# Kernel optimization log

Measured on AMD Instinct MI355X. Metric: run time of the kernel, lower is better.

Reference implementation:

```python
import jax, jax.numpy as jnp
import numpy as np
import math

N = 100000      # nodes
E = 1600000     # edges
D = 128         # in_channels
C = 256         # number of dominant-set cliques
HID = 64        # mlp_hidden
RATIO = 0.8
K = int(math.ceil(RATIO * N))  # 80000 topk nodes per view


def setup_inputs() -> dict:
    key = jax.random.key(0)
    ks = jax.random.split(key, 18)
    s = 0.05
    return {
        "x": jax.random.normal(ks[0], (N, D), jnp.float32),
        "edge_index": jax.random.randint(ks[1], (2, E), 0, N, dtype=jnp.int32),
        "batch": jnp.zeros((N,), jnp.int32),
        "cluster_id": jax.random.randint(ks[2], (N,), 0, C, dtype=jnp.int32),
        # MLP scorer: Linear(D,HID) -> ReLU -> Linear(HID,1)
        "mlp_w1": jax.random.normal(ks[3], (D, HID), jnp.float32) * s,
        "mlp_b1": jnp.zeros((HID,), jnp.float32),
        "mlp_w2": jax.random.normal(ks[4], (HID, 1), jnp.float32) * s,
        "mlp_b2": jnp.zeros((1,), jnp.float32),
        # GATConv(D, 1, heads=1)
        "gat_w": jax.random.normal(ks[5], (D, 1), jnp.float32) * s,
        "gat_a_src": jax.random.normal(ks[6], (1,), jnp.float32) * s,
        "gat_a_dst": jax.random.normal(ks[7], (1,), jnp.float32) * s,
        "gat_b": jnp.zeros((1,), jnp.float32),
        # InterChannelGCN attention Linear(2D,1) split into fine/coarse halves
        "att_w_fine": jax.random.normal(ks[8], (D,), jnp.float32) * s,
        "att_w_coarse": jax.random.normal(ks[9], (D,), jnp.float32) * s,
        "att_b": jnp.zeros((1,), jnp.float32),
        # InterChannelGCN transform Linear(D,D)
        "trans_w": jax.random.normal(ks[10], (D, D), jnp.float32) * s,
        "trans_b": jnp.zeros((D,), jnp.float32),
    }


def _inter_channel_gcn(h_fine, H_coarse, R, wa, wb, ab, tw, tb):
    # attention(Linear(2D,1)) on concat(h_fine_i, H_coarse_j) == h_fine@wa + H_coarse@wb + b
    scores = h_fine @ wa[:, None] + (H_coarse @ wb)[None, :] + ab[0]   # [K, C]
    attn = jax.nn.softmax(scores * R, axis=-1)                          # mask-by-multiply, as original
    out = attn @ H_coarse + h_fine                                      # add_self=True
    return jax.nn.relu(out @ tw + tb)                                   # normalize=False


def reference(x, edge_index, batch, cluster_id,
              mlp_w1, mlp_b1, mlp_w2, mlp_b2,
              gat_w, gat_a_src, gat_a_dst, gat_b,
              att_w_fine, att_w_coarse, att_b, trans_w, trans_b):
    src, dst = edge_index[0], edge_index[1]

    # --- DominantClustering('avg'): cluster means as coarse features ---
    counts = jax.ops.segment_sum(jnp.ones((N,), jnp.float32), cluster_id, num_segments=C)
    Hcoarse = jax.ops.segment_sum(x, cluster_id, num_segments=C) / jnp.maximum(counts, 1.0)[:, None]

    # --- feature view: MLP score + topk ---
    feature_score = (jax.nn.relu(x @ mlp_w1 + mlp_b1) @ mlp_w2 + mlp_b2)[:, 0]   # [N]
    _, feat_idx = jax.lax.top_k(feature_score, K)
    feature_view3 = x[feat_idx]
    R_feat = jax.nn.one_hot(cluster_id[feat_idx], C, dtype=x.dtype)              # relationship matrix
    fuse1 = _inter_channel_gcn(feature_view3, Hcoarse, R_feat,
                               att_w_fine, att_w_coarse, att_b, trans_w, trans_b)

    # --- local view: GATConv(D,1,heads=1) score + topk ---
    h = x @ gat_w                                                                 # [N,1]
    e = jax.nn.leaky_relu(gat_a_src[0] * h[src, 0] + gat_a_dst[0] * h[dst, 0], 0.2)  # [E]
    m = jax.ops.segment_max(e, dst, num_segments=N)
    ex = jnp.exp(e - m[dst])
    den = jax.ops.segment_sum(ex, dst, num_segments=N)
    alpha = ex / jnp.maximum(den[dst], 1e-16)
    localview_score = jax.ops.segment_sum(alpha * h[src, 0], dst, num_segments=N) + gat_b[0]
    _, local_idx = jax.lax.top_k(localview_score, K)
    local_view1 = x[local_idx]
    R_local = jax.nn.one_hot(cluster_id[local_idx], C, dtype=x.dtype)
    fuse2 = _inter_channel_gcn(local_view1, Hcoarse, R_local,
                               att_w_fine, att_w_coarse, att_b, trans_w, trans_b)

    # --- union, edge filtering + remapping (padded fixed shapes) ---
    in_feat = jnp.zeros((N,), bool).at[feat_idx].set(True)
    in_local = jnp.zeros((N,), bool).at[local_idx].set(True)
    union = in_feat | in_local
    mapping = jnp.where(union, jnp.cumsum(union.astype(jnp.int32)) - 1, -1)
    m0, m1 = mapping[src], mapping[dst]
    valid = (m0 >= 0) & (m1 >= 0)
    edge_index_topk = jnp.where(valid[None, :], jnp.stack([m0, m1]), -1)          # [2,E], -1 = dropped

    # --- fused features (faithful to original's fuse1/fuse2 index swap) ---
    A = jnp.zeros((N, D), x.dtype).at[feat_idx].set(fuse2)    # fuse2 indexed by feature topk position
    B = jnp.zeros((N, D), x.dtype).at[local_idx].set(fuse1)   # fuse1 indexed by local topk position
    both = in_feat & in_local
    Fp = jnp.where(both[:, None], (A + B) * 0.5, A + B)
    Fp = jnp.where(union[:, None], Fp, 0.0)                   # [N,D], zero outside union

    new_batch = jnp.where(union, batch, -1)
    return Fp, edge_index_topk, new_batch
```

## Files before the change

kernel.cpp:

```cpp
#include <hip/hip_runtime.h>
#include <hip/hip_bf16.h>
#include <stdint.h>

#define N 100000
#define E_ 1600000
#define D 128
#define C_ 256
#define HID 64
#define KSEL 80000
#define NB 4096
#define CHUNK 1024
#define NCHUNK ((N + CHUNK - 1) / CHUNK)
#define CSEG 32
#define NBK 782
#define BCAP 2560
#define RMAX 2048

__device__ __forceinline__ unsigned enc_f(float f) {
  unsigned b = __float_as_uint(f);
  return (b & 0x80000000u) ? ~b : (b | 0x80000000u);
}
__device__ __forceinline__ float dec_f(unsigned u) {
  unsigned b = (u & 0x80000000u) ? (u ^ 0x80000000u) : ~u;
  return __uint_as_float(b);
}

__global__ __launch_bounds__(256) void k_hist_cluster(const int* __restrict__ cid, int* __restrict__ ccount) {
  int n = blockIdx.x * 256 + threadIdx.x;
  if (n < N) atomicAdd(&ccount[cid[n]], 1);
}

__global__ __launch_bounds__(1024) void k_scan_small(const int* __restrict__ in0, int* __restrict__ out0, int n) {
  __shared__ int sums[1024];
  const int* in = in0 + (size_t)blockIdx.x * n;
  int* out = out0 + (size_t)blockIdx.x * n;
  int t = threadIdx.x;
  int per = (n + 1023) / 1024;
  int base = t * per;
  int loc = 0;
  for (int k = 0; k < per; ++k) { int i = base + k; if (i < n) loc += in[i]; }
  sums[t] = loc; __syncthreads();
  for (int off = 1; off < 1024; off <<= 1) {
    int v = (t >= off) ? sums[t - off] : 0;
    __syncthreads();
    sums[t] += v;
    __syncthreads();
  }
  int run = (t == 0) ? 0 : sums[t - 1];
  for (int k = 0; k < per; ++k) { int i = base + k; if (i < n) { out[i] = run; run += in[i]; } }
}

__global__ __launch_bounds__(256) void k_scatter_cluster(const int* __restrict__ cid, const int* __restrict__ cstart,
                                                         int* __restrict__ ccur, int* __restrict__ cslot) {
  int n = blockIdx.x * 256 + threadIdx.x;
  if (n < N) {
    int c = cid[n];
    int p = cstart[c] + atomicAdd(&ccur[c], 1);
    cslot[p] = n;
  }
}

__global__ __launch_bounds__(128) void k_cluster_partial(const float* __restrict__ x, const int* __restrict__ cstart,
                                                         const int* __restrict__ ccount, const int* __restrict__ cslot,
                                                         float* __restrict__ Hc) {
  int c = blockIdx.x >> 5;
  int s = blockIdx.x & (CSEG - 1);
  int d = threadIdx.x;
  int st = cstart[c], cnt = ccount[c];
  int seg = (cnt + CSEG - 1) / CSEG;
  int lo = s * seg;
  int hi = min(cnt, lo + seg);
  if (lo >= hi) return;
  float acc = 0.f;
  int k = lo;
  for (; k + 2 <= hi; k += 2) {
    int n0 = cslot[st + k], n1 = cslot[st + k + 1];
    float v0 = x[(size_t)n0 * D + d];
    float v1 = x[(size_t)n1 * D + d];
    acc += v0 + v1;
  }
  if (k < hi) acc += x[(size_t)cslot[st + k] * D + d];
  atomicAdd(&Hc[(size_t)c * D + d], acc);
}

__global__ __launch_bounds__(128) void k_mean_gdot(const int* __restrict__ ccount, const float* __restrict__ wb,
                                                   float* __restrict__ Hc, float* __restrict__ gdot) {
  __shared__ float red[128];
  int c = blockIdx.x, d = threadIdx.x;
  float hv = Hc[(size_t)c * D + d] / (float)max(ccount[c], 1);
  Hc[(size_t)c * D + d] = hv;
  red[d] = hv * wb[d];
  __syncthreads();
  if (d < 64) {
    float v = red[d] + red[d + 64];
    for (int off = 32; off; off >>= 1) v += __shfl_down(v, off);
    if (d == 0) gdot[c] = v;
  }
}

__global__ __launch_bounds__(128) void k_S_SW_HW(const float* __restrict__ Hc, const float* __restrict__ tw,
                                                 float* __restrict__ SW, float* __restrict__ HW) {
  __shared__ float Sl[128];
  int b = blockIdx.x, t = threadIdx.x;
  if (b == 0) {
    float s = 0.f;
    for (int c = 0; c < C_; ++c) s += Hc[(size_t)c * D + t];
    Sl[t] = s;
    __syncthreads();
    float acc = 0.f;
    for (int d = 0; d < D; ++d) acc = fmaf(Sl[d], tw[(size_t)d * D + t], acc);
    SW[t] = acc;
  } else {
    const float* src = Hc + (size_t)(b - 1) * D;
    float acc = 0.f;
    for (int d = 0; d < D; ++d) acc = fmaf(src[d], tw[(size_t)d * D + t], acc);
    HW[(size_t)(b - 1) * D + t] = acc;
  }
}

__global__ __launch_bounds__(256, 4) void k_score64(const float* __restrict__ x, const float* __restrict__ w1,
                                                    const float* __restrict__ b1, const float* __restrict__ w2,
                                                    const float* __restrict__ b2, const float* __restrict__ gw,
                                                    const float* __restrict__ wa, float* __restrict__ scoreF,
                                                    float* __restrict__ hg, float* __restrict__ aDot) {
  __shared__ float xld[64 * D];
  int tid = threadIdx.x;
  int base = blockIdx.x * 64;
#pragma unroll
  for (int k = 0; k < 8; ++k) {
    int i = k * 256 + tid;
    int r = i >> 5, off = i & 31;
    int n = base + r;
    float4 v = make_float4(0.f, 0.f, 0.f, 0.f);
    if (n < N) v = ((const float4*)(x + (size_t)n * D))[off];
    ((float4*)xld)[i] = v;
  }
  __syncthreads();

  int rg = tid >> 5;
  int cg = tid & 31;
  int c2 = cg * 2;
  float acc[8][2] = {};
  const float* xb = xld + rg * 8 * D;
  for (int d4 = 0; d4 < D; d4 += 4) {
    float2 wv0 = *(const float2*)(w1 + (size_t)(d4 + 0) * HID + c2);
    float2 wv1 = *(const float2*)(w1 + (size_t)(d4 + 1) * HID + c2);
    float2 wv2 = *(const float2*)(w1 + (size_t)(d4 + 2) * HID + c2);
    float2 wv3 = *(const float2*)(w1 + (size_t)(d4 + 3) * HID + c2);
#pragma unroll
    for (int r = 0; r < 8; ++r) {
      float4 xv = *(const float4*)(xb + r * D + d4);
      acc[r][0] = fmaf(xv.x, wv0.x, acc[r][0]);
      acc[r][1] = fmaf(xv.x, wv0.y, acc[r][1]);
      acc[r][0] = fmaf(xv.y, wv1.x, acc[r][0]);
      acc[r][1] = fmaf(xv.y, wv1.y, acc[r][1]);
      acc[r][0] = fmaf(xv.z, wv2.x, acc[r][0]);
      acc[r][1] = fmaf(xv.z, wv2.y, acc[r][1]);
      acc[r][0] = fmaf(xv.w, wv3.x, acc[r][0]);
      acc[r][1] = fmaf(xv.w, wv3.y, acc[r][1]);
    }
  }
  float2 b1v = *(const float2*)(b1 + c2);
  float2 w2v = *(const float2*)(w2 + c2);
  float bb = b2[0];
#pragma unroll
  for (int r = 0; r < 8; ++r) {
    float p = fmaxf(acc[r][0] + b1v.x, 0.f) * w2v.x + fmaxf(acc[r][1] + b1v.y, 0.f) * w2v.y;
#pragma unroll
    for (int off = 16; off; off >>= 1) p += __shfl_xor(p, off);
    if (cg == 0) {
      int n = base + rg * 8 + r;
      if (n < N) scoreF[n] = p + bb;
    }
  }
  float4 gwv = *(const float4*)(gw + cg * 4);
  float4 wav = *(const float4*)(wa + cg * 4);
#pragma unroll
  for (int r = 0; r < 8; ++r) {
    int row = rg * 8 + r;
    float4 xv = *(const float4*)(xld + row * D + cg * 4);
    float hp = xv.x * gwv.x + xv.y * gwv.y + xv.z * gwv.z + xv.w * gwv.w;
    float ap = xv.x * wav.x + xv.y * wav.y + xv.z * wav.z + xv.w * wav.w;
#pragma unroll
    for (int off = 16; off; off >>= 1) {
      hp += __shfl_xor(hp, off);
      ap += __shfl_xor(ap, off);
    }
    if (cg == 0) {
      int n = base + row;
      if (n < N) { hg[n] = hp; aDot[n] = ap; }
    }
  }
}

__global__ __launch_bounds__(1024) void k_escatter(const int* __restrict__ ei, const float* __restrict__ hg,
                                                   const float* __restrict__ asrc, const float* __restrict__ adst,
                                                   int* __restrict__ gcnt, uint2* __restrict__ payload) {
  __shared__ int lcnt[NBK];
  __shared__ int lbase[NBK];
  int tid = threadIdx.x;
  for (int i = tid; i < NBK; i += 1024) lcnt[i] = 0;
  int e0 = blockIdx.x * 8192;
  int es[8], ed[8];
#pragma unroll
  for (int k = 0; k < 8; ++k) {
    int e = e0 + k * 1024 + tid;
    bool v = (e < E_);
    es[k] = v ? ei[e] : -1;
    ed[k] = v ? ei[E_ + e] : -1;
  }
  __syncthreads();
#pragma unroll
  for (int k = 0; k < 8; ++k)
    if (ed[k] >= 0) atomicAdd(&lcnt[ed[k] >> 7], 1);
  __syncthreads();
  for (int i = tid; i < NBK; i += 1024) {
    int c = lcnt[i];
    lbase[i] = c ? atomicAdd(&gcnt[i], c) : 0;
    lcnt[i] = 0;
  }
  __syncthreads();
  float as = asrc[0], ad = adst[0];
#pragma unroll
  for (int k = 0; k < 8; ++k) {
    if (ed[k] < 0) continue;
    int s = es[k], d = ed[k];
    int b = d >> 7, dl = d & 127;
    float z = as * hg[s] + ad * hg[d];
    float ev = (z > 0.f) ? z : 0.2f * z;
    int pos = lbase[b] + atomicAdd(&lcnt[b], 1);
    if (pos < BCAP) {
      uint2 rec;
      rec.x = __float_as_uint(ev);
      rec.y = (unsigned)s | ((unsigned)dl << 24);
      payload[(size_t)b * BCAP + pos] = rec;
    }
  }
}

__global__ __launch_bounds__(256) void k_esoftmax(const uint2* __restrict__ payload, const int* __restrict__ gcnt,
                                                  const float* __restrict__ hg, const float* __restrict__ gb,
                                                  float* __restrict__ scoreL) {
  __shared__ unsigned mS[128];
  __shared__ float dS[128];
  __shared__ float nS[128];
  int b = blockIdx.x;
  int tid = threadIdx.x;
  if (tid < 128) { mS[tid] = 0u; dS[tid] = 0.f; nS[tid] = 0.f; }
  __syncthreads();
  int cnt = min(gcnt[b], BCAP);
  const uint2* bp = payload + (size_t)b * BCAP;
  for (int i = tid; i < cnt; i += 256) {
    uint2 r = bp[i];
    atomicMax(&mS[r.y >> 24], enc_f(__uint_as_float(r.x)));
  }
  __syncthreads();
  for (int i = tid; i < cnt; i += 256) {
    uint2 r = bp[i];
    int d = r.y >> 24;
    float ex = expf(__uint_as_float(r.x) - dec_f(mS[d]));
    atomicAdd(&dS[d], ex);
  }
  __syncthreads();
  for (int i = tid; i < cnt; i += 256) {
    uint2 r = bp[i];
    int d = r.y >> 24;
    float ex = expf(__uint_as_float(r.x) - dec_f(mS[d]));
    float alpha = ex / fmaxf(dS[d], 1e-16f);
    float h = hg[r.y & 0xFFFFFFu];
    atomicAdd(&nS[d], alpha * h);
  }
  __syncthreads();
  if (tid < 128) {
    int dst = b * 128 + tid;
    if (dst < N) scoreL[dst] = nS[tid] + gb[0];
  }
}

__global__ __launch_bounds__(256) void k_minmax2(const float* __restrict__ sc2, unsigned* __restrict__ mm) {
  __shared__ unsigned smx[256], smn[256];
  int v = blockIdx.y;
  const float* sc = sc2 + (size_t)v * N;
  int t = threadIdx.x; int n = blockIdx.x * 256 + t;
  unsigned val = (n < N) ? enc_f(sc[n]) : 0u;
  smx[t] = (n < N) ? val : 0u;
  smn[t] = (n < N) ? val : 0xFFFFFFFFu;
  __syncthreads();
  for (int off = 128; off; off >>= 1) {
    if (t < off) {
      smx[t] = max(smx[t], smx[t + off]);
      smn[t] = min(smn[t], smn[t + off]);
    }
    __syncthreads();
  }
  if (t == 0) { atomicMax(&mm[v], smx[0]); atomicMin(&mm[2 + v], smn[0]); }
}

__global__ __launch_bounds__(256) void k_bucket_hist2(const float* __restrict__ sc2, const unsigned* __restrict__ mm,
                                                      int* __restrict__ bucket2, int* __restrict__ hist2) {
  int v = blockIdx.y;
  int n = blockIdx.x * 256 + threadIdx.x;
  if (n >= N) return;
  const float* sc = sc2 + (size_t)v * N;
  float smax = dec_f(mm[v]), smin = dec_f(mm[2 + v]);
  float range = smax - smin;
  float scale = (range > 0.f) ? ((float)NB / range) : 0.f;
  float t = (smax - sc[n]) * scale;
  int b = (int)t;
  b = b < 0 ? 0 : (b > NB - 1 ? NB - 1 : b);
  bucket2[(size_t)v * N + n] = b;
  atomicAdd(&hist2[v * NB + b], 1);
}

__global__ __launch_bounds__(256) void k_bucket_scatter2(const int* __restrict__ bucket2, const int* __restrict__ start2,
                                                         int* __restrict__ cur2, int* __restrict__ slot2) {
  int v = blockIdx.y;
  int n = blockIdx.x * 256 + threadIdx.x;
  if (n >= N) return;
  int b = bucket2[(size_t)v * N + n];
  slot2[(size_t)v * N + start2[v * NB + b] + atomicAdd(&cur2[v * NB + b], 1)] = n;
}

__global__ __launch_bounds__(64) void k_bucket_rank3(const float* __restrict__ sc2, const int* __restrict__ start2,
                                                     const int* __restrict__ hist2, const int* __restrict__ slot2,
                                                     int* __restrict__ rank2, int* __restrict__ sorted2) {
  __shared__ unsigned long long keys[RMAX];
  int v = blockIdx.y;
  int b = blockIdx.x;
  int st = start2[v * NB + b], cnt = hist2[v * NB + b];
  if (cnt == 0) return;
  const float* sc = sc2 + (size_t)v * N;
  const int* slot = slot2 + (size_t)v * N;
  int* rank = rank2 + (size_t)v * N;
  int* sorted = sorted2 + (size_t)v * N;
  int tid = threadIdx.x;
  if (cnt <= RMAX) {
    for (int i = tid; i < cnt; i += 64) {
      int m = slot[st + i];
      keys[i] = (((unsigned long long)(~enc_f(sc[m]))) << 32) | (unsigned)m;
    }
    __syncthreads();
    for (int i = tid; i < cnt; i += 64) {
      unsigned long long mykey = keys[i];
      int r = 0;
      for (int j = 0; j < cnt; ++j) r += (keys[j] < mykey) ? 1 : 0;
      int m = (int)(mykey & 0xFFFFFFFFu);
      rank[m] = st + r;
      sorted[st + r] = m;
    }
  } else {
    for (int i = tid; i < cnt; i += 64) {
      int m = slot[st + i];
      unsigned long long mykey = (((unsigned long long)(~enc_f(sc[m]))) << 32) | (unsigned)m;
      int r = 0;
      for (int j = 0; j < cnt; ++j) {
        int mj = slot[st + j];
        unsigned long long k = (((unsigned long long)(~enc_f(sc[mj]))) << 32) | (unsigned)mj;
        r += (k < mykey) ? 1 : 0;
      }
      rank[m] = st + r;
      sorted[st + r] = m;
    }
  }
}

__global__ __launch_bounds__(1024) void k_union_chunksum(const int* __restrict__ rankF, const int* __restrict__ rankL,
                                                         int* __restrict__ csum) {
  __shared__ int red[1024];
  int t = threadIdx.x; int i = blockIdx.x * 1024 + t;
  int u = (i < N) ? (((rankF[i] < KSEL) || (rankL[i] < KSEL)) ? 1 : 0) : 0;
  red[t] = u; __syncthreads();
  for (int off = 512; off; off >>= 1) { if (t < off) red[t] += red[t + off]; __syncthreads(); }
  if (t == 0) csum[blockIdx.x] = red[0];
}

__global__ __launch_bounds__(1024) void k_union_map(const int* __restrict__ rankF, const int* __restrict__ rankL,
                                                    const int* __restrict__ cstart, const int* __restrict__ batch,
                                                    int* __restrict__ mapping, float* __restrict__ outBatch) {
  __shared__ int sums[1024];
  int t = threadIdx.x; int i = blockIdx.x * 1024 + t;
  int u = (i < N) ? (((rankF[i] < KSEL) || (rankL[i] < KSEL)) ? 1 : 0) : 0;
  sums[t] = u; __syncthreads();
  for (int off = 1; off < 1024; off <<= 1) {
    int v = (t >= off) ? sums[t - off] : 0;
    __syncthreads();
    sums[t] += v;
    __syncthreads();
  }
  if (i < N) {
    mapping[i] = u ? (cstart[blockIdx.x] + sums[t] - 1) : -1;
    outBatch[i] = u ? (float)batch[i] : -1.0f;
  }
}

__global__ __launch_bounds__(256) void k_edge_out(const int* __restrict__ ei, const int* __restrict__ mapping,
                                                  float* __restrict__ outE) {
  int e = blockIdx.x * 256 + threadIdx.x;
  if (e >= E_) return;
  int m0 = mapping[ei[e]], m1 = mapping[ei[E_ + e]];
  bool valid = (m0 >= 0) && (m1 >= 0);
  outE[e] = valid ? (float)m0 : -1.f;
  outE[E_ + e] = valid ? (float)m1 : -1.f;
}

__global__ __launch_bounds__(128, 2) void k_fuse64(const float* __restrict__ x, const float* __restrict__ tw,
                                                   const float* __restrict__ tb, const float* __restrict__ SW,
                                                   const float* __restrict__ HW, const float* __restrict__ gdot,
                                                   const float* __restrict__ aDot, const int* __restrict__ cid,
                                                   const int* __restrict__ srcL, const int* __restrict__ tgtL,
                                                   const float* __restrict__ attb, const int* __restrict__ rankF,
                                                   float* __restrict__ Fp, int accum) {
  __shared__ float xld[64 * D];
  __shared__ float pq[64 * 2];
  __shared__ int mt[64 * 2];
  int tid = threadIdx.x;
  int base = blockIdx.x * 64;
  if (tid < 64) {
    int ws = srcL[base + tid];
    int cc = cid[ws];
    mt[tid * 2] = cc;
    mt[tid * 2 + 1] = tgtL[base + tid];
    float s = aDot[ws] + gdot[cc] + attb[0];
    float mx = fmaxf(s, 0.f);
    float esm = expf(s - mx), eom = expf(-mx);
    float dn = esm + 255.f * eom;
    pq[tid * 2] = esm / dn;
    pq[tid * 2 + 1] = eom / dn;
  }
#pragma unroll
  for (int k = 0; k < 16; ++k) {
    int i = k * 128 + tid;
    int r = i >> 5, off = i & 31;
    int ws = srcL[base + r];
    ((float4*)xld)[i] = ((const float4*)(x + (size_t)ws * D))[off];
  }
  __syncthreads();

  int rg = tid >> 4;
  int cg = tid & 15;
  int c8 = cg * 8;
  float acc[8][8] = {};
  const float* xb = xld + rg * 8 * D;
  for (int d4 = 0; d4 < D; d4 += 4) {
    float tww[4][8];
#pragma unroll
    for (int dd = 0; dd < 4; ++dd) {
      *(float4*)&tww[dd][0] = *(const float4*)(tw + (size_t)(d4 + dd) * D + c8);
      *(float4*)&tww[dd][4] = *(const float4*)(tw + (size_t)(d4 + dd) * D + c8 + 4);
    }
#pragma unroll
    for (int r = 0; r < 8; ++r) {
      float4 xv = *(const float4*)(xb + r * D + d4);
      float xs[4] = {xv.x, xv.y, xv.z, xv.w};
#pragma unroll
      for (int dd = 0; dd < 4; ++dd)
#pragma unroll
        for (int c = 0; c < 8; ++c)
          acc[r][c] = fmaf(xs[dd], tww[dd][c], acc[r][c]);
    }
  }

  float4 tb0 = *(const float4*)(tb + c8);
  float4 tb1 = *(const float4*)(tb + c8 + 4);
  float4 sw0 = *(const float4*)(SW + c8);
  float4 sw1 = *(const float4*)(SW + c8 + 4);
#pragma unroll
  for (int r = 0; r < 8; ++r) {
    int row = rg * 8 + r;
    float p = pq[row * 2], q = pq[row * 2 + 1];
    int cc = mt[row * 2];
    int tgt = mt[row * 2 + 1];
    float4 hw0 = *(const float4*)(HW + (size_t)cc * D + c8);
    float4 hw1 = *(const float4*)(HW + (size_t)cc * D + c8 + 4);
    float4 o0, o1;
    o0.x = fmaxf(acc[r][0] + tb0.x + q * sw0.x + (p - q) * hw0.x, 0.f);
    o0.y = fmaxf(acc[r][1] + tb0.y + q * sw0.y + (p - q) * hw0.y, 0.f);
    o0.z = fmaxf(acc[r][2] + tb0.z + q * sw0.z + (p - q) * hw0.z, 0.f);
    o0.w = fmaxf(acc[r][3] + tb0.w + q * sw0.w + (p - q) * hw0.w, 0.f);
    o1.x = fmaxf(acc[r][4] + tb1.x + q * sw1.x + (p - q) * hw1.x, 0.f);
    o1.y = fmaxf(acc[r][5] + tb1.y + q * sw1.y + (p - q) * hw1.y, 0.f);
    o1.z = fmaxf(acc[r][6] + tb1.z + q * sw1.z + (p - q) * hw1.z, 0.f);
    o1.w = fmaxf(acc[r][7] + tb1.w + q * sw1.w + (p - q) * hw1.w, 0.f);
    float4* dst0 = (float4*)(Fp + (size_t)tgt * D + c8);
    float4* dst1 = (float4*)(Fp + (size_t)tgt * D + c8 + 4);
    if (accum) {
      float4 a0 = *dst0, a1 = *dst1;
      o0.x += a0.x; o0.y += a0.y; o0.z += a0.z; o0.w += a0.w;
      o1.x += a1.x; o1.y += a1.y; o1.z += a1.z; o1.w += a1.w;
      if (rankF[tgt] < KSEL) {
        o0.x *= 0.5f; o0.y *= 0.5f; o0.z *= 0.5f; o0.w *= 0.5f;
        o1.x *= 0.5f; o1.y *= 0.5f; o1.z *= 0.5f; o1.w *= 0.5f;
      }
    }
    *dst0 = o0;
    *dst1 = o1;
  }
}

extern "C" void kernel_launch(void* const* d_in, const int* in_sizes, int n_in,
                              void* d_out, int out_size, void* d_ws, size_t ws_size,
                              hipStream_t stream) {
  const float* x   = (const float*)d_in[0];
  const int* ei    = (const int*)d_in[1];
  const int* batch = (const int*)d_in[2];
  const int* cid   = (const int*)d_in[3];
  const float* w1  = (const float*)d_in[4];
  const float* b1  = (const float*)d_in[5];
  const float* w2  = (const float*)d_in[6];
  const float* b2  = (const float*)d_in[7];
  const float* gw  = (const float*)d_in[8];
  const float* gas = (const float*)d_in[9];
  const float* gad = (const float*)d_in[10];
  const float* gb  = (const float*)d_in[11];
  const float* wa  = (const float*)d_in[12];
  const float* wb  = (const float*)d_in[13];
  const float* ab  = (const float*)d_in[14];
  const float* tw  = (const float*)d_in[15];
  const float* tb  = (const float*)d_in[16];
  (void)in_sizes; (void)n_in; (void)ws_size; (void)out_size;

  char* p = (char*)d_ws;
  auto alloc = [&](size_t bytes) -> char* {
    char* r = p;
    p += (bytes + 255) & ~(size_t)255;
    return r;
  };
  int* ccount    = (int*)alloc(C_ * 4);
  int* ccur      = (int*)alloc(C_ * 4);
  unsigned* mm   = (unsigned*)alloc(16);
  int* hist2     = (int*)alloc(2 * NB * 4);
  int* cur2      = (int*)alloc(2 * NB * 4);
  float* Hc      = (float*)alloc((size_t)C_ * D * 4);
  int* gcnt      = (int*)alloc(NBK * 4);
  size_t zeroBytes = (size_t)(p - (char*)d_ws);
  int* cstart   = (int*)alloc(C_ * 4);
  int* cslot    = (int*)alloc((size_t)N * 4);
  float* gdot   = (float*)alloc(C_ * 4);
  float* SW     = (float*)alloc(D * 4);
  float* HW     = (float*)alloc((size_t)C_ * D * 4);
  float* score2 = (float*)alloc((size_t)2 * N * 4);
  float* hg     = (float*)alloc((size_t)N * 4);
  float* aDot   = (float*)alloc((size_t)N * 4);
  uint2* payload = (uint2*)alloc((size_t)NBK * BCAP * 8);
  int* bucket2  = (int*)alloc((size_t)2 * N * 4);
  int* start2   = (int*)alloc(2 * NB * 4);
  int* slot2    = (int*)alloc((size_t)2 * N * 4);
  int* sorted2  = (int*)alloc((size_t)2 * N * 4);
  int* rank2    = (int*)alloc((size_t)2 * N * 4);
  int* csums    = (int*)alloc(NCHUNK * 4);
  int* cstarts  = (int*)alloc(NCHUNK * 4);
  int* mapping  = (int*)alloc((size_t)N * 4);

  float* scoreF = score2;
  float* scoreL = score2 + N;
  int* sortedF  = sorted2;
  int* sortedL  = sorted2 + N;
  int* rankF    = rank2;
  int* rankL    = rank2 + N;

  float* outF = (float*)d_out;
  float* outE = outF + (size_t)N * D;
  float* outB = outE + (size_t)2 * E_;

  hipMemsetAsync(d_ws, 0, zeroBytes, stream);
  hipMemsetAsync(outF, 0, (size_t)N * D * 4, stream);
  hipMemsetAsync(mm + 2, 0xFF, 8, stream);

  k_hist_cluster<<<(N + 255) / 256, 256, 0, stream>>>(cid, ccount);
  k_scan_small<<<1, 1024, 0, stream>>>(ccount, cstart, C_);
  k_scatter_cluster<<<(N + 255) / 256, 256, 0, stream>>>(cid, cstart, ccur, cslot);
  k_cluster_partial<<<C_ * CSEG, 128, 0, stream>>>(x, cstart, ccount, cslot, Hc);
  k_mean_gdot<<<C_, 128, 0, stream>>>(ccount, wb, Hc, gdot);
  k_S_SW_HW<<<C_ + 1, 128, 0, stream>>>(Hc, tw, SW, HW);

  k_score64<<<(N + 63) / 64, 256, 0, stream>>>(x, w1, b1, w2, b2, gw, wa, scoreF, hg, aDot);
  k_escatter<<<(E_ + 8191) / 8192, 1024, 0, stream>>>(ei, hg, gas, gad, gcnt, payload);
  k_esoftmax<<<NBK, 256, 0, stream>>>(payload, gcnt, hg, gb, scoreL);

  dim3 g2((N + 255) / 256, 2);
  k_minmax2<<<g2, 256, 0, stream>>>(score2, mm);
  k_bucket_hist2<<<g2, 256, 0, stream>>>(score2, mm, bucket2, hist2);
  k_scan_small<<<2, 1024, 0, stream>>>(hist2, start2, NB);
  k_bucket_scatter2<<<g2, 256, 0, stream>>>(bucket2, start2, cur2, slot2);
  dim3 gr(NB, 2);
  k_bucket_rank3<<<gr, 64, 0, stream>>>(score2, start2, hist2, slot2, rank2, sorted2);

  k_union_chunksum<<<NCHUNK, 1024, 0, stream>>>(rankF, rankL, csums);
  k_scan_small<<<1, 1024, 0, stream>>>(csums, cstarts, NCHUNK);
  k_union_map<<<NCHUNK, 1024, 0, stream>>>(rankF, rankL, cstarts, batch, mapping, outB);
  k_edge_out<<<(E_ + 255) / 256, 256, 0, stream>>>(ei, mapping, outE);

  k_fuse64<<<KSEL / 64, 128, 0, stream>>>(x, tw, tb, SW, HW, gdot, aDot, cid, sortedL, sortedF, ab, rankF, outF, 0);
  k_fuse64<<<KSEL / 64, 128, 0, stream>>>(x, tw, tb, SW, HW, gdot, aDot, cid, sortedF, sortedL, ab, rankF, outF, 1);
}
```

Before: 589.2 us.

## Zero only non-union rows and retile fuse kernel to 256 threads

The full memset of the feature output is replaced by a small kernel that zeroes only rows outside the union, since union rows are fully overwritten by the two fuse passes. The second fuse pass now reads back the previous row only for nodes present in both views, and precomputes that flag in shared memory. The fuse GEMM moves from 128 threads with 8x8 tiles to 256 threads with 8x4 tiles, with register double-buffering of the transform weights. This saves output bandwidth but adds a launch, and the smaller tiles load the weights more times per output.

```diff
diff --git a/kernel.cpp b/kernel.cpp
--- a/kernel.cpp
+++ b/kernel.cpp
@@ -403,7 +403,13 @@
   outE[E_ + e] = valid ? (float)m1 : -1.f;
 }
 
-__global__ __launch_bounds__(128, 2) void k_fuse64(const float* __restrict__ x, const float* __restrict__ tw,
+__global__ __launch_bounds__(256) void k_zero_rows(const int* __restrict__ mapping, float* __restrict__ Fp) {
+  int i = blockIdx.x * 256 + threadIdx.x;
+  int n = i >> 5;
+  if (n < N && mapping[n] < 0) ((float4*)Fp)[i] = make_float4(0.f, 0.f, 0.f, 0.f);
+}
+
+__global__ __launch_bounds__(256, 4) void k_fuse64(const float* __restrict__ x, const float* __restrict__ tw,
                                                    const float* __restrict__ tb, const float* __restrict__ SW,
                                                    const float* __restrict__ HW, const float* __restrict__ gdot,
                                                    const float* __restrict__ aDot, const int* __restrict__ cid,
@@ -413,13 +419,16 @@
   __shared__ float xld[64 * D];
   __shared__ float pq[64 * 2];
   __shared__ int mt[64 * 2];
+  __shared__ int ft[64];
   int tid = threadIdx.x;
   int base = blockIdx.x * 64;
   if (tid < 64) {
     int ws = srcL[base + tid];
     int cc = cid[ws];
+    int tg = tgtL[base + tid];
     mt[tid * 2] = cc;
-    mt[tid * 2 + 1] = tgtL[base + tid];
+    mt[tid * 2 + 1] = tg;
+    ft[tid] = (rankF[tg] < KSEL) ? 1 : 0;
     float s = aDot[ws] + gdot[cc] + attb[0];
     float mx = fmaxf(s, 0.f);
     float esm = expf(s - mx), eom = expf(-mx);
@@ -428,72 +437,78 @@
     pq[tid * 2 + 1] = eom / dn;
   }
 #pragma unroll
-  for (int k = 0; k < 16; ++k) {
-    int i = k * 128 + tid;
+  for (int k = 0; k < 8; ++k) {
+    int i = k * 256 + tid;
     int r = i >> 5, off = i & 31;
     int ws = srcL[base + r];
     ((float4*)xld)[i] = ((const float4*)(x + (size_t)ws * D))[off];
   }
   __syncthreads();
 
-  int rg = tid >> 4;
-  int cg = tid & 15;
-  int c8 = cg * 8;
-  float acc[8][8] = {};
+  int rg = tid >> 5;
+  int c4 = (tid & 31) * 4;
+  float acc[8][4] = {};
   const float* xb = xld + rg * 8 * D;
+  float4 t0 = *(const float4*)(tw + (size_t)0 * D + c4);
+  float4 t1 = *(const float4*)(tw + (size_t)1 * D + c4);
+  float4 t2 = *(const float4*)(tw + (size_t)2 * D + c4);
+  float4 t3 = *(const float4*)(tw + (size_t)3 * D + c4);
   for (int d4 = 0; d4 < D; d4 += 4) {
-    float tww[4][8];
-#pragma unroll
-    for (int dd = 0; dd < 4; ++dd) {
-      *(float4*)&tww[dd][0] = *(const float4*)(tw + (size_t)(d4 + dd) * D + c8);
-      *(float4*)&tww[dd][4] = *(const float4*)(tw + (size_t)(d4 + dd) * D + c8 + 4);
+    float4 u0, u1, u2, u3;
+    if (d4 + 4 < D) {
+      u0 = *(const float4*)(tw + (size_t)(d4 + 4) * D + c4);
+      u1 = *(const float4*)(tw + (size_t)(d4 + 5) * D + c4);
+      u2 = *(const float4*)(tw + (size_t)(d4 + 6) * D + c4);
+      u3 = *(const float4*)(tw + (size_t)(d4 + 7) * D + c4);
+    } else {
+      u0 = u1 = u2 = u3 = make_float4(0.f, 0.f, 0.f, 0.f);
     }
 #pragma unroll
     for (int r = 0; r < 8; ++r) {
       float4 xv = *(const float4*)(xb + r * D + d4);
-      float xs[4] = {xv.x, xv.y, xv.z, xv.w};
-#pragma unroll
-      for (int dd = 0; dd < 4; ++dd)
-#pragma unroll
-        for (int c = 0; c < 8; ++c)
-          acc[r][c] = fmaf(xs[dd], tww[dd][c], acc[r][c]);
-    }
-  }
-
-  float4 tb0 = *(const float4*)(tb + c8);
-  float4 tb1 = *(const float4*)(tb + c8 + 4);
-  float4 sw0 = *(const float4*)(SW + c8);
-  float4 sw1 = *(const float4*)(SW + c8 + 4);
+      acc[r][0] = fmaf(xv.x, t0.x, acc[r][0]);
+      acc[r][1] = fmaf(xv.x, t0.y, acc[r][1]);
+      acc[r][2] = fmaf(xv.x, t0.z, acc[r][2]);
+      acc[r][3] = fmaf(xv.x, t0.w, acc[r][3]);
+      acc[r][0] = fmaf(xv.y, t1.x, acc[r][0]);
+      acc[r][1] = fmaf(xv.y, t1.y, acc[r][1]);
+      acc[r][2] = fmaf(xv.y, t1.z, acc[r][2]);
+      acc[r][3] = fmaf(xv.y, t1.w, acc[r][3]);
+      acc[r][0] = fmaf(xv.z, t2.x, acc[r][0]);
+      acc[r][1] = fmaf(xv.z, t2.y, acc[r][1]);
+      acc[r][2] = fmaf(xv.z, t2.z, acc[r][2]);
+      acc[r][3] = fmaf(xv.z, t2.w, acc[r][3]);
+      acc[r][0] = fmaf(xv.w, t3.x, acc[r][0]);
+      acc[r][1] = fmaf(xv.w, t3.y, acc[r][1]);
+      acc[r][2] = fmaf(xv.w, t3.z, acc[r][2]);
+      acc[r][3] = fmaf(xv.w, t3.w, acc[r][3]);
+    }
+    t0 = u0; t1 = u1; t2 = u2; t3 = u3;
+  }
+
+  float4 tbv = *(const float4*)(tb + c4);
+  float4 swv = *(const float4*)(SW + c4);
 #pragma unroll
   for (int r = 0; r < 8; ++r) {
     int row = rg * 8 + r;
     float p = pq[row * 2], q = pq[row * 2 + 1];
     int cc = mt[row * 2];
     int tgt = mt[row * 2 + 1];
-    float4 hw0 = *(const float4*)(HW + (size_t)cc * D + c8);
-    float4 hw1 = *(const float4*)(HW + (size_t)cc * D + c8 + 4);
-    float4 o0, o1;
-    o0.x = fmaxf(acc[r][0] + tb0.x + q * sw0.x + (p - q) * hw0.x, 0.f);
-    o0.y = fmaxf(acc[r][1] + tb0.y + q * sw0.y + (p - q) * hw0.y, 0.f);
-    o0.z = fmaxf(acc[r][2] + tb0.z + q * sw0.z + (p - q) * hw0.z, 0.f);
-    o0.w = fmaxf(acc[r][3] + tb0.w + q * sw0.w + (p - q) * hw0.w, 0.f);
-    o1.x = fmaxf(acc[r][4] + tb1.x + q * sw1.x + (p - q) * hw1.x, 0.f);
-    o1.y = fmaxf(acc[r][5] + tb1.y + q * sw1.y + (p - q) * hw1.y, 0.f);
-    o1.z = fmaxf(acc[r][6] + tb1.z + q * sw1.z + (p - q) * hw1.z, 0.f);
-    o1.w = fmaxf(acc[r][7] + tb1.w + q * sw1.w + (p - q) * hw1.w, 0.f);
-    float4* dst0 = (float4*)(Fp + (size_t)tgt * D + c8);
-    float4* dst1 = (float4*)(Fp + (size_t)tgt * D + c8 + 4);
-    if (accum) {
-      float4 a0 = *dst0, a1 = *dst1;
-      o0.x += a0.x; o0.y += a0.y; o0.z += a0.z; o0.w += a0.w;
-      o1.x += a1.x; o1.y += a1.y; o1.z += a1.z; o1.w += a1.w;
-      if (rankF[tgt] < KSEL) {
-        o0.x *= 0.5f; o0.y *= 0.5f; o0.z *= 0.5f; o0.w *= 0.5f;
-        o1.x *= 0.5f; o1.y *= 0.5f; o1.z *= 0.5f; o1.w *= 0.5f;
-      }
-    }
-    *dst0 = o0;
-    *dst1 = o1;
+    float4 hw = *(const float4*)(HW + (size_t)cc * D + c4);
+    float4 o;
+    o.x = fmaxf(acc[r][0] + tbv.x + q * swv.x + (p - q) * hw.x, 0.f);
+    o.y = fmaxf(acc[r][1] + tbv.y + q * swv.y + (p - q) * hw.y, 0.f);
+    o.z = fmaxf(acc[r][2] + tbv.z + q * swv.z + (p - q) * hw.z, 0.f);
+    o.w = fmaxf(acc[r][3] + tbv.w + q * swv.w + (p - q) * hw.w, 0.f);
+    float4* dst = (float4*)(Fp + (size_t)tgt * D + c4);
+    if (accum && ft[row]) {
+      float4 old = *dst;
+      o.x = (o.x + old.x) * 0.5f;
+      o.y = (o.y + old.y) * 0.5f;
+      o.z = (o.z + old.z) * 0.5f;
+      o.w = (o.w + old.w) * 0.5f;
+    }
+    *dst = o;
   }
 }
 
@@ -563,7 +578,6 @@
   float* outB = outE + (size_t)2 * E_;
 
   hipMemsetAsync(d_ws, 0, zeroBytes, stream);
-  hipMemsetAsync(outF, 0, (size_t)N * D * 4, stream);
   hipMemsetAsync(mm + 2, 0xFF, 8, stream);
 
   k_hist_cluster<<<(N + 255) / 256, 256, 0, stream>>>(cid, ccount);
@@ -589,7 +603,8 @@
   k_scan_small<<<1, 1024, 0, stream>>>(csums, cstarts, NCHUNK);
   k_union_map<<<NCHUNK, 1024, 0, stream>>>(rankF, rankL, cstarts, batch, mapping, outB);
   k_edge_out<<<(E_ + 255) / 256, 256, 0, stream>>>(ei, mapping, outE);
-
-  k_fuse64<<<KSEL / 64, 128, 0, stream>>>(x, tw, tb, SW, HW, gdot, aDot, cid, sortedL, sortedF, ab, rankF, outF, 0);
-  k_fuse64<<<KSEL / 64, 128, 0, stream>>>(x, tw, tb, SW, HW, gdot, aDot, cid, sortedF, sortedL, ab, rankF, outF, 1);
-}
+  k_zero_rows<<<(N * 32 + 255) / 256, 256, 0, stream>>>(mapping, outF);
+
+  k_fuse64<<<KSEL / 64, 256, 0, stream>>>(x, tw, tb, SW, HW, gdot, aDot, cid, sortedL, sortedF, ab, rankF, outF, 0);
+  k_fuse64<<<KSEL / 64, 256, 0, stream>>>(x, tw, tb, SW, HW, gdot, aDot, cid, sortedF, sortedL, ab, rankF, outF, 1);
+}
```

After: 578.9 us. No clear change (-1.8%).
